# Performance work log

Measured on AMD Instinct MI355X. Metric: run time of the kernel, lower is better.

Reference implementation:

```python
import jax, jax.numpy as jnp
import numpy as np

HEADS = 7
DIM_HEAD = 64
SCALE = DIM_HEAD ** -0.5


def setup_inputs() -> dict:
    key = jax.random.key(0)
    ks = jax.random.split(key, 6)
    b, n, dim = 8, 1024, 448
    inner = HEADS * DIM_HEAD  # 448
    x = jax.random.normal(ks[0], (b, n, dim), dtype=jnp.float32)
    w_qv = jax.random.normal(ks[1], (dim, 2 * inner), dtype=jnp.float32) * 0.02
    ext_k = jax.random.normal(ks[2], (HEADS, n, DIM_HEAD), dtype=jnp.float32)
    ext_bias = jax.random.normal(ks[3], (HEADS, n, n), dtype=jnp.float32)
    w_out = jax.random.normal(ks[4], (inner, dim), dtype=jnp.float32) * 0.02
    b_out = jnp.zeros((dim,), dtype=jnp.float32)
    return {"x": x, "w_qv": w_qv, "ext_k": ext_k, "ext_bias": ext_bias,
            "w_out": w_out, "b_out": b_out}


def reference(x, w_qv, ext_k, ext_bias, w_out, b_out):
    b, n, dim = x.shape
    qv = x @ w_qv                                   # [b, n, 2*inner]
    q, v = jnp.split(qv, 2, axis=-1)
    # b n (h d) -> b h n d
    q = q.reshape(b, n, HEADS, DIM_HEAD).transpose(0, 2, 1, 3)
    v = v.reshape(b, n, HEADS, DIM_HEAD).transpose(0, 2, 1, 3)
    # scores vs external learned key, additive bias applied BEFORE scale
    dots = (jnp.einsum('bhnd,hmd->bhnm', q, ext_k) + ext_bias[None]) * SCALE
    attn = jax.nn.softmax(dots, axis=-1)
    out = jnp.einsum('bhnm,bhmd->bhnd', attn, v)
    out = out.transpose(0, 2, 1, 3).reshape(b, n, HEADS * DIM_HEAD)
    return out @ w_out + b_out  # dropout is identity in eval mode
```

## Files before the change

### kernel.cpp

```cpp
#include <hip/hip_runtime.h>
#include <hip/hip_bf16.h>
#include <hip/hip_fp16.h>

#define BATCH 8
#define NSEQ 1024
#define DIMM 448
#define NHEAD 7
#define HDIM 64
#define MROWS (BATCH*NSEQ)
#define KDIM 448
#define SCALE_F 0.125f

typedef short short8 __attribute__((ext_vector_type(8)));
typedef float floatx16 __attribute__((ext_vector_type(16)));

#define MFMA32(a,b,c) __builtin_amdgcn_mfma_f32_32x32x16_bf16(a,b,c,0,0,0)

__device__ __forceinline__ unsigned short f2bf(float f){
    __hip_bfloat16 h = __float2bfloat16(f);
    return *reinterpret_cast<unsigned short*>(&h);
}
__device__ __forceinline__ float bf2f(unsigned short u){
    __hip_bfloat16 h; *reinterpret_cast<unsigned short*>(&h) = u;
    return __bfloat162float(h);
}
__device__ __forceinline__ float h2f(unsigned short u){
    __half h; *reinterpret_cast<unsigned short*>(&h) = u;
    return __half2float(h);
}
__device__ __forceinline__ unsigned short f2h(float f){
    __half h = __float2half(f);
    return *reinterpret_cast<unsigned short*>(&h);
}

__global__ __launch_bounds__(256)
void prep_all(const float* __restrict__ x, const float* __restrict__ ek,
              const float* __restrict__ wqv, const float* __restrict__ wout,
              const float* __restrict__ eb,
              unsigned short* __restrict__ xh, unsigned short* __restrict__ ekh,
              unsigned short* __restrict__ wqvTh, unsigned short* __restrict__ woTh,
              unsigned short* __restrict__ woTl, unsigned short* __restrict__ bp)
{
    __shared__ float T[2][64][33];
    const int bx = blockIdx.x, tid = threadIdx.x;

    if (bx < 3584) {
        int i = bx*256 + tid;
        float4 v = ((const float4*)x)[i];
        ((ushort4*)xh)[i] = make_ushort4(f2bf(v.x), f2bf(v.y), f2bf(v.z), f2bf(v.w));
    } else if (bx < 4032) {
        int i = (bx-3584)*256 + tid;
        float4 v = ((const float4*)ek)[i];
        ((ushort4*)ekh)[i] = make_ushort4(f2bf(v.x), f2bf(v.y), f2bf(v.z), f2bf(v.w));
    } else if (bx < 4228) {
        int lid = (bx-4032)*4 + (tid>>6);
        int kc = lid % 56, ng = lid / 56;
        int n = ng*64 + (tid&63);
        unsigned short h[8];
#pragma unroll
        for (int j = 0; j < 8; ++j) h[j] = f2bf(wqv[(size_t)(kc*8+j)*896 + n]);
        size_t o = (size_t)n*KDIM + kc*8;
        *(ushort4*)(wqvTh + o)     = make_ushort4(h[0],h[1],h[2],h[3]);
        *(ushort4*)(wqvTh + o + 4) = make_ushort4(h[4],h[5],h[6],h[7]);
    } else if (bx < 4340) {
        int lid = (bx-4228)*4 + (tid>>6);
        int kc = lid % 56, ng = lid / 56;
        int n = ng*64 + (tid&63);
        ushort4 h0={0,0,0,0}, h1={0,0,0,0}, l0={0,0,0,0}, l1={0,0,0,0};
        if (n < DIMM) {
            unsigned short h[8], l[8];
#pragma unroll
            for (int j = 0; j < 8; ++j) {
                float f = wout[(size_t)(kc*8+j)*DIMM + n];
                h[j] = f2bf(f); l[j] = f2bf(f - bf2f(h[j]));
            }
            h0 = make_ushort4(h[0],h[1],h[2],h[3]); h1 = make_ushort4(h[4],h[5],h[6],h[7]);
            l0 = make_ushort4(l[0],l[1],l[2],l[3]); l1 = make_ushort4(l[4],l[5],l[6],l[7]);
        }
        size_t o = (size_t)n*KDIM + kc*8;
        *(ushort4*)(woTh + o) = h0; *(ushort4*)(woTh + o + 4) = h1;
        *(ushort4*)(woTl + o) = l0; *(ushort4*)(woTl + o + 4) = l1;
    } else {
        const int sub = tid >> 7, st = tid & 127;
        const int lid = (bx-4340)*2 + sub;
        const int mt = lid & 31, qt = (lid>>5) & 15, h = lid >> 9;
#pragma unroll
        for (int it = 0; it < 4; ++it) {
            int idx = it*128 + st;
            int row = idx >> 3, c4 = (idx & 7)*4;
            float4 v = *(const float4*)(eb + ((size_t)(h*NSEQ + qt*64 + row))*NSEQ + mt*32 + c4);
            T[sub][row][c4+0]=v.x; T[sub][row][c4+1]=v.y;
            T[sub][row][c4+2]=v.z; T[sub][row][c4+3]=v.w;
        }
        __syncthreads();
        const int g2 = st >> 6, lane = st & 63;
        const int lq = lane & 31, quad = lane >> 5;
        const int q = g2*32 + lq;
        unsigned short* dst = bp + ((((size_t)h*16 + qt)*32 + mt)*4 + g2*2)*512 + lane*8;
#pragma unroll
        for (int jj = 0; jj < 2; ++jj) {
            unsigned short o[8];
#pragma unroll
            for (int t = 0; t < 8; ++t) {
                int m = (t&3) + 8*(t>>2) + 16*jj + 4*quad;
                o[t] = f2h(T[sub][q][m] * SCALE_F);
            }
            *(ushort4*)(dst + jj*512)     = make_ushort4(o[0],o[1],o[2],o[3]);
            *(ushort4*)(dst + jj*512 + 4) = make_ushort4(o[4],o[5],o[6],o[7]);
        }
    }
}

__global__ __launch_bounds__(64, 2)
void gemm1_reg(const unsigned short* __restrict__ Ah, const unsigned short* __restrict__ Bh,
               unsigned short* __restrict__ qd, unsigned short* __restrict__ vTd)
{
    const int lane = threadIdx.x;
    const int lq = lane & 31, lh = lane >> 5;
    const int m0 = blockIdx.x * 64;
    const int y  = blockIdx.y;
    const int n0 = y * 64;
    const unsigned short* aB = Ah + (size_t)(m0 + lq)*KDIM + lh*8;
    const unsigned short* bB = Bh + (size_t)(n0 + lq)*KDIM + lh*8;

    floatx16 acc[2][2] = {};
    short8 aR[2][2][2], bR[2][2][2];
#define LD1(kt, par) {                                                        \
    _Pragma("unroll") for (int fm = 0; fm < 2; ++fm)                          \
    _Pragma("unroll") for (int c = 0; c < 2; ++c) {                           \
        aR[par][fm][c] = *(const short8*)(aB + (size_t)fm*32*KDIM + (kt)*32 + c*16); \
        bR[par][fm][c] = *(const short8*)(bB + (size_t)fm*32*KDIM + (kt)*32 + c*16); } }

    LD1(0, 0)
#pragma unroll
    for (int kt = 0; kt < 14; ++kt) {
        const int par = kt & 1;
        if (kt < 13) LD1(kt+1, par^1)
#pragma unroll
        for (int c = 0; c < 2; ++c)
#pragma unroll
            for (int fm = 0; fm < 2; ++fm)
#pragma unroll
                for (int fn = 0; fn < 2; ++fn)
                    acc[fm][fn] = MFMA32(aR[par][fm][c], bR[par][fn][c], acc[fm][fn]);
    }
#undef LD1

    if (y < NHEAD) {
#pragma unroll
        for (int fm = 0; fm < 2; ++fm)
#pragma unroll
            for (int fn = 0; fn < 2; ++fn) {
                const int d = fn*32 + lq;
#pragma unroll
                for (int r = 0; r < 16; ++r) {
                    const int gm = m0 + fm*32 + (r&3) + 8*(r>>2) + 4*lh;
                    const int b = gm >> 10, ns = gm & 1023;
                    qd[((size_t)((b*NHEAD + y)*NSEQ + ns))*HDIM + d] = f2bf(acc[fm][fn][r]);
                }
            }
    } else {
        const int head = y - NHEAD;
#pragma unroll
        for (int fm = 0; fm < 2; ++fm)
#pragma unroll
            for (int fn = 0; fn < 2; ++fn) {
                const int d = fn*32 + lq;
#pragma unroll
                for (int r = 0; r < 16; ++r) {
                    const int gm = m0 + fm*32 + (r&3) + 8*(r>>2) + 4*lh;
                    const int b = gm >> 10, ns = gm & 1023;
                    vTd[((size_t)((b*NHEAD + head)*HDIM + d))*NSEQ + ns] = f2bf(acc[fm][fn][r]);
                }
            }
    }
}

__global__ __launch_bounds__(64, 2)
void attn4(const unsigned short* __restrict__ qh_g, const unsigned short* __restrict__ vTh,
           const unsigned short* __restrict__ ekh, const unsigned short* __restrict__ bp,
           unsigned short* __restrict__ aoh, unsigned short* __restrict__ aol)
{
    __shared__ unsigned short pS[1024];
    __shared__ float linv[2][32];

    const int lane = threadIdx.x;
    const int lq = lane & 31, lh = lane >> 5;
    const int qt = blockIdx.x, head = blockIdx.y, b = blockIdx.z;
    const int bh = b*NHEAD + head;

    short8 qf[2][4];
#pragma unroll
    for (int g2 = 0; g2 < 2; ++g2)
#pragma unroll
        for (int c = 0; c < 4; ++c)
            qf[g2][c] = *(const short8*)(qh_g +
                ((size_t)(bh*NSEQ) + qt*64 + g2*32 + lq)*HDIM + c*16 + lh*8);

    const unsigned short* kB = ekh + ((size_t)head*NSEQ + lq)*HDIM + lh*8;
    const unsigned short* vB = vTh + ((size_t)(bh*HDIM) + lq)*NSEQ;
    const unsigned short* bB = bp + ((size_t)(head*16 + qt))*65536 + lane*8;

    short8 kR[2][4], vR[2][4], bR[2][4];
#define PREF(J, par) { const int mm = ((J) < 32) ? (J) : 0;                    \
    _Pragma("unroll") for (int c = 0; c < 4; ++c)                              \
        kR[par][c] = *(const short8*)(kB + (size_t)mm*2048 + c*16);            \
    _Pragma("unroll") for (int c2 = 0; c2 < 2; ++c2)                           \
    _Pragma("unroll") for (int h2 = 0; h2 < 2; ++h2)                           \
        vR[par][c2*2+h2] = *(const short8*)(vB + (size_t)(h2*32)*NSEQ + mm*32 + (c2*2+lh)*8); \
    _Pragma("unroll") for (int u = 0; u < 4; ++u)                              \
        bR[par][u] = *(const short8*)(bB + ((size_t)mm*4 + u)*512); }

    floatx16 O[2][2] = {};
    float ls[2] = {0.f, 0.f};

#define SEC(J, par, nxt) {                                                     \
    PREF((J)+1, nxt)                                                           \
    _Pragma("unroll") for (int g2 = 0; g2 < 2; ++g2) {                         \
        floatx16 S = {};                                                       \
        _Pragma("unroll") for (int c = 0; c < 4; ++c)                          \
            S = MFMA32(kR[par][c], qf[g2][c], S);                              \
        _Pragma("unroll") for (int g = 0; g < 4; ++g) {                        \
            unsigned short hb[4];                                              \
            _Pragma("unroll") for (int j2 = 0; j2 < 4; ++j2) {                 \
                const int i = g*4 + j2;                                        \
                float bs = h2f((unsigned short)bR[par][g2*2 + (i>>3)][i&7]);   \
                float pv = __expf(fmaf(S[i], SCALE_F, bs));                    \
                ls[g2] += pv;  hb[j2] = f2bf(pv);                              \
            }                                                                  \
            *(ushort4*)(pS + g*256 + lq*8 + lh*4) = make_ushort4(hb[0],hb[1],hb[2],hb[3]); \
        }                                                                      \
        _Pragma("unroll") for (int c2 = 0; c2 < 2; ++c2) {                     \
            short8 pf = *(const short8*)(pS + ((c2*2+lh)*32 + lq)*8);          \
            O[g2][0] = MFMA32(pf, vR[par][c2*2+0], O[g2][0]);                  \
            O[g2][1] = MFMA32(pf, vR[par][c2*2+1], O[g2][1]);                  \
        } } }

    PREF(0, 0)
    for (int jj = 0; jj < 16; ++jj) {
        SEC(2*jj,   0, 1)
        SEC(2*jj+1, 1, 0)
    }
#undef SEC
#undef PREF

    float lt0 = ls[0] + __shfl_xor(ls[0], 32);
    float lt1 = ls[1] + __shfl_xor(ls[1], 32);
    if (lh == 0) { linv[0][lq] = 1.f/lt0; linv[1][lq] = 1.f/lt1; }

#pragma unroll
    for (int g2 = 0; g2 < 2; ++g2)
#pragma unroll
        for (int r = 0; r < 16; ++r) {
            const int qr = (r&3) + 8*(r>>2) + 4*lh;
            const float inv = linv[g2][qr];
            const size_t o = ((size_t)(b*NSEQ) + qt*64 + g2*32 + qr)*DIMM + head*HDIM + lq;
            float v0 = O[g2][0][r]*inv, v1 = O[g2][1][r]*inv;
            unsigned short h0 = f2bf(v0), h1 = f2bf(v1);
            aoh[o]      = h0;  aol[o]      = f2bf(v0 - bf2f(h0));
            aoh[o + 32] = h1;  aol[o + 32] = f2bf(v1 - bf2f(h1));
        }
}

__global__ __launch_bounds__(64, 2)
void gemm2_reg(const unsigned short* __restrict__ Ah, const unsigned short* __restrict__ Al,
               const unsigned short* __restrict__ Bh, const unsigned short* __restrict__ Bl,
               const float* __restrict__ bias, float* __restrict__ out)
{
    const int lane = threadIdx.x;
    const int lq = lane & 31, lh = lane >> 5;
    const int m0 = blockIdx.x * 64;
    const int n0 = blockIdx.y * 64;
    const unsigned short* aBh = Ah + (size_t)(m0 + lq)*KDIM + lh*8;
    const unsigned short* aBl = Al + (size_t)(m0 + lq)*KDIM + lh*8;
    const unsigned short* bBh = Bh + (size_t)(n0 + lq)*KDIM + lh*8;
    const unsigned short* bBl = Bl + (size_t)(n0 + lq)*KDIM + lh*8;

    floatx16 acc[2][2] = {};
    short8 aH[2][2][2], aL[2][2][2], bH[2][2][2], bL[2][2][2];
#define LD2(kt, par) {                                                        \
    _Pragma("unroll") for (int fm = 0; fm < 2; ++fm)                          \
    _Pragma("unroll") for (int c = 0; c < 2; ++c) {                           \
        const size_t off = (size_t)fm*32*KDIM + (kt)*32 + c*16;               \
        aH[par][fm][c] = *(const short8*)(aBh + off);                         \
        aL[par][fm][c] = *(const short8*)(aBl + off);                         \
        bH[par][fm][c] = *(const short8*)(bBh + off);                         \
        bL[par][fm][c] = *(const short8*)(bBl + off); } }

    LD2(0, 0)
#pragma unroll
    for (int kt = 0; kt < 14; ++kt) {
        const int par = kt & 1;
        if (kt < 13) LD2(kt+1, par^1)
#pragma unroll
        for (int c = 0; c < 2; ++c)
#pragma unroll
            for (int fm = 0; fm < 2; ++fm)
#pragma unroll
                for (int fn = 0; fn < 2; ++fn) {
                    acc[fm][fn] = MFMA32(aH[par][fm][c], bH[par][fn][c], acc[fm][fn]);
                    acc[fm][fn] = MFMA32(aL[par][fm][c], bH[par][fn][c], acc[fm][fn]);
                    acc[fm][fn] = MFMA32(aH[par][fm][c], bL[par][fn][c], acc[fm][fn]);
                }
    }
#undef LD2

#pragma unroll
    for (int fm = 0; fm < 2; ++fm)
#pragma unroll
        for (int fn = 0; fn < 2; ++fn) {
            const int gn = n0 + fn*32 + lq;
            const float bv = bias[gn];
#pragma unroll
            for (int r = 0; r < 16; ++r) {
                const int gm = m0 + fm*32 + (r&3) + 8*(r>>2) + 4*lh;
                out[(size_t)gm*DIMM + gn] = acc[fm][fn][r] + bv;
            }
        }
}

extern "C" void kernel_launch(void* const* d_in, const int* in_sizes, int n_in,
                              void* d_out, int out_size, void* d_ws, size_t ws_size,
                              hipStream_t stream)
{
    const float* x    = (const float*)d_in[0];
    const float* wqv  = (const float*)d_in[1];
    const float* ek   = (const float*)d_in[2];
    const float* eb   = (const float*)d_in[3];
    const float* wout = (const float*)d_in[4];
    const float* bout = (const float*)d_in[5];
    float* out = (float*)d_out;

    const size_t MK = (size_t)MROWS*KDIM;
    const size_t EK = (size_t)NHEAD*NSEQ*HDIM;
    unsigned short* p = (unsigned short*)d_ws;
    unsigned short* xh    = p;  p += MK;
    unsigned short* wqvTh = p;  p += (size_t)896*KDIM;
    unsigned short* woTh  = p;  p += (size_t)512*KDIM;
    unsigned short* woTl  = p;  p += (size_t)512*KDIM;
    unsigned short* ekh   = p;  p += EK;
    unsigned short* qh    = p;  p += MK;
    unsigned short* vTh   = p;  p += MK;
    unsigned short* bp    = p;  p += (size_t)NHEAD*NSEQ*NSEQ;
    unsigned short* aoh   = p;  p += MK;
    unsigned short* aol   = p;  p += MK;

    prep_all<<<6132, 256, 0, stream>>>(x, ek, wqv, wout, eb,
                                       xh, ekh, wqvTh, woTh, woTl, bp);
    gemm1_reg<<<dim3(128, 14), 64, 0, stream>>>(xh, wqvTh, qh, vTh);
    attn4<<<dim3(16, NHEAD, BATCH), 64, 0, stream>>>(qh, vTh, ekh, bp, aoh, aol);
    gemm2_reg<<<dim3(128, 7), 64, 0, stream>>>(aoh, aol, woTh, woTl, bout, out);
}
```

Baseline: 200.6 us.

## Rewrite pipeline: fuse bias prepack and x conversion, batch-share bias in attention

Drops the separate fp16 repacking pass over the large bias tensor and the x-to-bf16 conversion. gemm1 now converts fp32 x on the fly and prescales q by scale*log2e. The attention kernel puts all 8 batches of one head in a single 512-thread block so each bias row is read once from fp32 memory and shared across batches. It also uses exp2 and moves P between lane halves with cross-lane shuffles instead of shared memory. Both GEMMs move to 4-wave 128x128 tiles, which trades occupancy and adds padding waste in gemm2 (448 columns do not fill 4x128).

```diff
diff --git a/kernel.cpp b/kernel.cpp
--- a/kernel.cpp
+++ b/kernel.cpp
@@ -1,6 +1,5 @@
 #include <hip/hip_runtime.h>
 #include <hip/hip_bf16.h>
-#include <hip/hip_fp16.h>
 
 #define BATCH 8
 #define NSEQ 1024
@@ -9,10 +8,12 @@
 #define HDIM 64
 #define MROWS (BATCH*NSEQ)
 #define KDIM 448
-#define SCALE_F 0.125f
+#define CB 0.18033688f
 
 typedef short short8 __attribute__((ext_vector_type(8)));
+typedef int   int4v  __attribute__((ext_vector_type(4)));
 typedef float floatx16 __attribute__((ext_vector_type(16)));
+typedef unsigned int u32;
 
 #define MFMA32(a,b,c) __builtin_amdgcn_mfma_f32_32x32x16_bf16(a,b,c,0,0,0)
 
@@ -24,36 +25,23 @@
     __hip_bfloat16 h; *reinterpret_cast<unsigned short*>(&h) = u;
     return __bfloat162float(h);
 }
-__device__ __forceinline__ float h2f(unsigned short u){
-    __half h; *reinterpret_cast<unsigned short*>(&h) = u;
-    return __half2float(h);
-}
-__device__ __forceinline__ unsigned short f2h(float f){
-    __half h = __float2half(f);
-    return *reinterpret_cast<unsigned short*>(&h);
+__device__ __forceinline__ short8 i4_to_s8(int4v v){
+    union { int4v i; short8 s; } u; u.i = v; return u.s;
 }
 
 __global__ __launch_bounds__(256)
-void prep_all(const float* __restrict__ x, const float* __restrict__ ek,
-              const float* __restrict__ wqv, const float* __restrict__ wout,
-              const float* __restrict__ eb,
-              unsigned short* __restrict__ xh, unsigned short* __restrict__ ekh,
-              unsigned short* __restrict__ wqvTh, unsigned short* __restrict__ woTh,
-              unsigned short* __restrict__ woTl, unsigned short* __restrict__ bp)
-{
-    __shared__ float T[2][64][33];
+void prep_r8(const float* __restrict__ ek, const float* __restrict__ wqv,
+             const float* __restrict__ wout,
+             unsigned short* __restrict__ ekh, unsigned short* __restrict__ wqvTh,
+             unsigned short* __restrict__ woTh, unsigned short* __restrict__ woTl)
+{
     const int bx = blockIdx.x, tid = threadIdx.x;
-
-    if (bx < 3584) {
+    if (bx < 448) {
         int i = bx*256 + tid;
-        float4 v = ((const float4*)x)[i];
-        ((ushort4*)xh)[i] = make_ushort4(f2bf(v.x), f2bf(v.y), f2bf(v.z), f2bf(v.w));
-    } else if (bx < 4032) {
-        int i = (bx-3584)*256 + tid;
         float4 v = ((const float4*)ek)[i];
         ((ushort4*)ekh)[i] = make_ushort4(f2bf(v.x), f2bf(v.y), f2bf(v.z), f2bf(v.w));
-    } else if (bx < 4228) {
-        int lid = (bx-4032)*4 + (tid>>6);
+    } else if (bx < 644) {
+        int lid = (bx-448)*4 + (tid>>6);
         int kc = lid % 56, ng = lid / 56;
         int n = ng*64 + (tid&63);
         unsigned short h[8];
@@ -62,8 +50,8 @@
         size_t o = (size_t)n*KDIM + kc*8;
         *(ushort4*)(wqvTh + o)     = make_ushort4(h[0],h[1],h[2],h[3]);
         *(ushort4*)(wqvTh + o + 4) = make_ushort4(h[4],h[5],h[6],h[7]);
-    } else if (bx < 4340) {
-        int lid = (bx-4228)*4 + (tid>>6);
+    } else {
+        int lid = (bx-644)*4 + (tid>>6);
         int kc = lid % 56, ng = lid / 56;
         int n = ng*64 + (tid&63);
         ushort4 h0={0,0,0,0}, h1={0,0,0,0}, l0={0,0,0,0}, l1={0,0,0,0};
@@ -80,163 +68,140 @@
         size_t o = (size_t)n*KDIM + kc*8;
         *(ushort4*)(woTh + o) = h0; *(ushort4*)(woTh + o + 4) = h1;
         *(ushort4*)(woTl + o) = l0; *(ushort4*)(woTl + o + 4) = l1;
-    } else {
-        const int sub = tid >> 7, st = tid & 127;
-        const int lid = (bx-4340)*2 + sub;
-        const int mt = lid & 31, qt = (lid>>5) & 15, h = lid >> 9;
-#pragma unroll
-        for (int it = 0; it < 4; ++it) {
-            int idx = it*128 + st;
-            int row = idx >> 3, c4 = (idx & 7)*4;
-            float4 v = *(const float4*)(eb + ((size_t)(h*NSEQ + qt*64 + row))*NSEQ + mt*32 + c4);
-            T[sub][row][c4+0]=v.x; T[sub][row][c4+1]=v.y;
-            T[sub][row][c4+2]=v.z; T[sub][row][c4+3]=v.w;
+    }
+}
+
+__global__ __launch_bounds__(256, 2)
+void gemm1_r8(const float* __restrict__ x, const unsigned short* __restrict__ Bh,
+              unsigned short* __restrict__ qd, unsigned short* __restrict__ vTd)
+{
+    const int tid = threadIdx.x, w = tid >> 6, lane = tid & 63;
+    const int lq = lane & 31, lh = lane >> 5;
+    const int m0 = blockIdx.x*128 + w*32, n0 = blockIdx.y*128;
+    const float* aB = x + (size_t)(m0 + lq)*KDIM + lh*8;
+    const unsigned short* bB = Bh + (size_t)(n0 + lq)*KDIM + lh*8;
+
+    floatx16 acc[4] = {};
+    float4 aF[2][2][2];
+    short8 bR[2][8];
+#define LD1(kt, sl) {                                                          \
+    _Pragma("unroll") for (int c = 0; c < 2; ++c) {                            \
+        aF[sl][c][0] = *(const float4*)(aB + (kt)*32 + c*16);                  \
+        aF[sl][c][1] = *(const float4*)(aB + (kt)*32 + c*16 + 4);              \
+        _Pragma("unroll") for (int fn = 0; fn < 4; ++fn)                       \
+            bR[sl][fn*2+c] = *(const short8*)(bB + (size_t)(fn*32)*KDIM + (kt)*32 + c*16); } }
+
+    LD1(0, 0)
+#pragma unroll
+    for (int kt = 0; kt < 14; ++kt) {
+        if (kt < 13) LD1(kt+1, (kt+1)&1)
+        const int sl = kt & 1;
+#pragma unroll
+        for (int c = 0; c < 2; ++c) {
+            float4 f0 = aF[sl][c][0], f1 = aF[sl][c][1];
+            short8 a;
+            a[0]=(short)f2bf(f0.x); a[1]=(short)f2bf(f0.y);
+            a[2]=(short)f2bf(f0.z); a[3]=(short)f2bf(f0.w);
+            a[4]=(short)f2bf(f1.x); a[5]=(short)f2bf(f1.y);
+            a[6]=(short)f2bf(f1.z); a[7]=(short)f2bf(f1.w);
+#pragma unroll
+            for (int fn = 0; fn < 4; ++fn)
+                acc[fn] = MFMA32(a, bR[sl][fn*2+c], acc[fn]);
         }
-        __syncthreads();
-        const int g2 = st >> 6, lane = st & 63;
-        const int lq = lane & 31, quad = lane >> 5;
-        const int q = g2*32 + lq;
-        unsigned short* dst = bp + ((((size_t)h*16 + qt)*32 + mt)*4 + g2*2)*512 + lane*8;
-#pragma unroll
-        for (int jj = 0; jj < 2; ++jj) {
-            unsigned short o[8];
-#pragma unroll
-            for (int t = 0; t < 8; ++t) {
-                int m = (t&3) + 8*(t>>2) + 16*jj + 4*quad;
-                o[t] = f2h(T[sub][q][m] * SCALE_F);
-            }
-            *(ushort4*)(dst + jj*512)     = make_ushort4(o[0],o[1],o[2],o[3]);
-            *(ushort4*)(dst + jj*512 + 4) = make_ushort4(o[4],o[5],o[6],o[7]);
+    }
+#undef LD1
+
+#pragma unroll
+    for (int fn = 0; fn < 4; ++fn) {
+        const int gn = n0 + fn*32 + lq;
+        const int hcol = gn >> 6, d = gn & 63;
+#pragma unroll
+        for (int r = 0; r < 16; ++r) {
+            const int gm = m0 + (r&3) + 8*(r>>2) + 4*lh;
+            const int b = gm >> 10, ns = gm & 1023;
+            if (hcol < NHEAD)
+                qd[((size_t)((b*NHEAD + hcol)*NSEQ + ns))*HDIM + d] = f2bf(acc[fn][r]*CB);
+            else
+                vTd[((size_t)((b*NHEAD + hcol - NHEAD)*HDIM + d))*NSEQ + ns] = f2bf(acc[fn][r]);
         }
     }
 }
 
-__global__ __launch_bounds__(64, 2)
-void gemm1_reg(const unsigned short* __restrict__ Ah, const unsigned short* __restrict__ Bh,
-               unsigned short* __restrict__ qd, unsigned short* __restrict__ vTd)
-{
-    const int lane = threadIdx.x;
+__global__ __launch_bounds__(512, 2)
+void attn6(const unsigned short* __restrict__ qh_g, const unsigned short* __restrict__ vTh,
+           const unsigned short* __restrict__ ekh, const float* __restrict__ eb,
+           unsigned short* __restrict__ aoh, unsigned short* __restrict__ aol)
+{
+    __shared__ float linv[8][32];
+
+    const int tid = threadIdx.x;
+    const int w = tid >> 6;
+    const int lane = tid & 63;
     const int lq = lane & 31, lh = lane >> 5;
-    const int m0 = blockIdx.x * 64;
-    const int y  = blockIdx.y;
-    const int n0 = y * 64;
-    const unsigned short* aB = Ah + (size_t)(m0 + lq)*KDIM + lh*8;
-    const unsigned short* bB = Bh + (size_t)(n0 + lq)*KDIM + lh*8;
-
-    floatx16 acc[2][2] = {};
-    short8 aR[2][2][2], bR[2][2][2];
-#define LD1(kt, par) {                                                        \
-    _Pragma("unroll") for (int fm = 0; fm < 2; ++fm)                          \
-    _Pragma("unroll") for (int c = 0; c < 2; ++c) {                           \
-        aR[par][fm][c] = *(const short8*)(aB + (size_t)fm*32*KDIM + (kt)*32 + c*16); \
-        bR[par][fm][c] = *(const short8*)(bB + (size_t)fm*32*KDIM + (kt)*32 + c*16); } }
-
-    LD1(0, 0)
-#pragma unroll
-    for (int kt = 0; kt < 14; ++kt) {
-        const int par = kt & 1;
-        if (kt < 13) LD1(kt+1, par^1)
-#pragma unroll
-        for (int c = 0; c < 2; ++c)
-#pragma unroll
-            for (int fm = 0; fm < 2; ++fm)
-#pragma unroll
-                for (int fn = 0; fn < 2; ++fn)
-                    acc[fm][fn] = MFMA32(aR[par][fm][c], bR[par][fn][c], acc[fm][fn]);
-    }
-#undef LD1
-
-    if (y < NHEAD) {
-#pragma unroll
-        for (int fm = 0; fm < 2; ++fm)
-#pragma unroll
-            for (int fn = 0; fn < 2; ++fn) {
-                const int d = fn*32 + lq;
-#pragma unroll
-                for (int r = 0; r < 16; ++r) {
-                    const int gm = m0 + fm*32 + (r&3) + 8*(r>>2) + 4*lh;
-                    const int b = gm >> 10, ns = gm & 1023;
-                    qd[((size_t)((b*NHEAD + y)*NSEQ + ns))*HDIM + d] = f2bf(acc[fm][fn][r]);
-                }
-            }
-    } else {
-        const int head = y - NHEAD;
-#pragma unroll
-        for (int fm = 0; fm < 2; ++fm)
-#pragma unroll
-            for (int fn = 0; fn < 2; ++fn) {
-                const int d = fn*32 + lq;
-#pragma unroll
-                for (int r = 0; r < 16; ++r) {
-                    const int gm = m0 + fm*32 + (r&3) + 8*(r>>2) + 4*lh;
-                    const int b = gm >> 10, ns = gm & 1023;
-                    vTd[((size_t)((b*NHEAD + head)*HDIM + d))*NSEQ + ns] = f2bf(acc[fm][fn][r]);
-                }
-            }
-    }
-}
-
-__global__ __launch_bounds__(64, 2)
-void attn4(const unsigned short* __restrict__ qh_g, const unsigned short* __restrict__ vTh,
-           const unsigned short* __restrict__ ekh, const unsigned short* __restrict__ bp,
-           unsigned short* __restrict__ aoh, unsigned short* __restrict__ aol)
-{
-    __shared__ unsigned short pS[1024];
-    __shared__ float linv[2][32];
-
-    const int lane = threadIdx.x;
-    const int lq = lane & 31, lh = lane >> 5;
-    const int qt = blockIdx.x, head = blockIdx.y, b = blockIdx.z;
-    const int bh = b*NHEAD + head;
-
-    short8 qf[2][4];
-#pragma unroll
-    for (int g2 = 0; g2 < 2; ++g2)
-#pragma unroll
-        for (int c = 0; c < 4; ++c)
-            qf[g2][c] = *(const short8*)(qh_g +
-                ((size_t)(bh*NSEQ) + qt*64 + g2*32 + lq)*HDIM + c*16 + lh*8);
-
-    const unsigned short* kB = ekh + ((size_t)head*NSEQ + lq)*HDIM + lh*8;
+    const int qt = blockIdx.x, h = blockIdx.y;
+    const int bh = w*NHEAD + h;
+
+    short8 qf[4];
+#pragma unroll
+    for (int c = 0; c < 4; ++c)
+        qf[c] = *(const short8*)(qh_g +
+            ((size_t)(bh*NSEQ) + qt*32 + lq)*HDIM + c*16 + lh*8);
+
+    const unsigned short* kB = ekh + ((size_t)h*NSEQ + lq)*HDIM + lh*8;
     const unsigned short* vB = vTh + ((size_t)(bh*HDIM) + lq)*NSEQ;
-    const unsigned short* bB = bp + ((size_t)(head*16 + qt))*65536 + lane*8;
-
-    short8 kR[2][4], vR[2][4], bR[2][4];
-#define PREF(J, par) { const int mm = ((J) < 32) ? (J) : 0;                    \
+    const float* bB = eb + ((size_t)(h*NSEQ) + qt*32 + lq)*NSEQ;
+
+    short8 kR[2][4], vR[2][4];
+    float4 bR[2][4];
+#define PREF(MM, SL) {                                                         \
     _Pragma("unroll") for (int c = 0; c < 4; ++c)                              \
-        kR[par][c] = *(const short8*)(kB + (size_t)mm*2048 + c*16);            \
+        kR[SL][c] = *(const short8*)(kB + (size_t)(MM)*2048 + c*16);           \
+    _Pragma("unroll") for (int fn = 0; fn < 2; ++fn)                           \
     _Pragma("unroll") for (int c2 = 0; c2 < 2; ++c2)                           \
-    _Pragma("unroll") for (int h2 = 0; h2 < 2; ++h2)                           \
-        vR[par][c2*2+h2] = *(const short8*)(vB + (size_t)(h2*32)*NSEQ + mm*32 + (c2*2+lh)*8); \
-    _Pragma("unroll") for (int u = 0; u < 4; ++u)                              \
-        bR[par][u] = *(const short8*)(bB + ((size_t)mm*4 + u)*512); }
-
-    floatx16 O[2][2] = {};
-    float ls[2] = {0.f, 0.f};
-
-#define SEC(J, par, nxt) {                                                     \
-    PREF((J)+1, nxt)                                                           \
-    _Pragma("unroll") for (int g2 = 0; g2 < 2; ++g2) {                         \
-        floatx16 S = {};                                                       \
-        _Pragma("unroll") for (int c = 0; c < 4; ++c)                          \
-            S = MFMA32(kR[par][c], qf[g2][c], S);                              \
-        _Pragma("unroll") for (int g = 0; g < 4; ++g) {                        \
-            unsigned short hb[4];                                              \
-            _Pragma("unroll") for (int j2 = 0; j2 < 4; ++j2) {                 \
-                const int i = g*4 + j2;                                        \
-                float bs = h2f((unsigned short)bR[par][g2*2 + (i>>3)][i&7]);   \
-                float pv = __expf(fmaf(S[i], SCALE_F, bs));                    \
-                ls[g2] += pv;  hb[j2] = f2bf(pv);                              \
-            }                                                                  \
-            *(ushort4*)(pS + g*256 + lq*8 + lh*4) = make_ushort4(hb[0],hb[1],hb[2],hb[3]); \
+        vR[SL][fn*2+c2] = __builtin_nontemporal_load(                          \
+            (const short8*)(vB + (size_t)(fn*32)*NSEQ + (MM)*32 + c2*16 + lh*8)); \
+    _Pragma("unroll") for (int g = 0; g < 4; ++g)                              \
+        bR[SL][g] = *(const float4*)(bB + (size_t)(MM)*32 + g*8 + lh*4); }
+
+    floatx16 O[2] = {};
+    float ls = 0.f;
+
+#define SEC(J, PAR, NXT) {                                                     \
+    { const int mm_ = ((J)+1 < 32) ? (J)+1 : 0; PREF(mm_, NXT) }               \
+    floatx16 S = {};                                                           \
+    S = MFMA32(kR[PAR][0], qf[0], S);                                          \
+    S = MFMA32(kR[PAR][1], qf[1], S);                                          \
+    S = MFMA32(kR[PAR][2], qf[2], S);                                          \
+    S = MFMA32(kR[PAR][3], qf[3], S);                                          \
+    u32 Pq[4][2];                                                              \
+    _Pragma("unroll") for (int g = 0; g < 4; ++g) {                            \
+        float bvv[4] = {bR[PAR][g].x, bR[PAR][g].y, bR[PAR][g].z, bR[PAR][g].w}; \
+        unsigned short hb[4];                                                  \
+        _Pragma("unroll") for (int j = 0; j < 4; ++j) {                        \
+            float pv = __builtin_amdgcn_exp2f(fmaf(bvv[j], CB, S[g*4+j]));     \
+            ls += pv;  hb[j] = f2bf(pv);                                       \
         }                                                                      \
-        _Pragma("unroll") for (int c2 = 0; c2 < 2; ++c2) {                     \
-            short8 pf = *(const short8*)(pS + ((c2*2+lh)*32 + lq)*8);          \
-            O[g2][0] = MFMA32(pf, vR[par][c2*2+0], O[g2][0]);                  \
-            O[g2][1] = MFMA32(pf, vR[par][c2*2+1], O[g2][1]);                  \
-        } } }
+        Pq[g][0] = (u32)hb[0] | ((u32)hb[1] << 16);                            \
+        Pq[g][1] = (u32)hb[2] | ((u32)hb[3] << 16);                            \
+    }                                                                          \
+    u32 pp[4][2];                                                              \
+    _Pragma("unroll") for (int g = 0; g < 4; ++g) {                            \
+        pp[g][0] = (u32)__shfl_xor((int)Pq[g][0], 32);                         \
+        pp[g][1] = (u32)__shfl_xor((int)Pq[g][1], 32);                         \
+    }                                                                          \
+    _Pragma("unroll") for (int c2 = 0; c2 < 2; ++c2) {                         \
+        int4v iv;                                                              \
+        iv.x = lh ? (int)pp[2*c2+1][0] : (int)Pq[2*c2][0];                     \
+        iv.y = lh ? (int)pp[2*c2+1][1] : (int)Pq[2*c2][1];                     \
+        iv.z = lh ? (int)Pq[2*c2+1][0] : (int)pp[2*c2][0];                     \
+        iv.w = lh ? (int)Pq[2*c2+1][1] : (int)pp[2*c2][1];                     \
+        short8 af = i4_to_s8(iv);                                              \
+        O[0] = MFMA32(af, vR[PAR][0*2+c2], O[0]);                              \
+        O[1] = MFMA32(af, vR[PAR][1*2+c2], O[1]);                              \
+    } }
 
     PREF(0, 0)
+#pragma unroll
     for (int jj = 0; jj < 16; ++jj) {
         SEC(2*jj,   0, 1)
         SEC(2*jj+1, 1, 0)
@@ -244,79 +209,73 @@
 #undef SEC
 #undef PREF
 
-    float lt0 = ls[0] + __shfl_xor(ls[0], 32);
-    float lt1 = ls[1] + __shfl_xor(ls[1], 32);
-    if (lh == 0) { linv[0][lq] = 1.f/lt0; linv[1][lq] = 1.f/lt1; }
-
-#pragma unroll
-    for (int g2 = 0; g2 < 2; ++g2)
-#pragma unroll
-        for (int r = 0; r < 16; ++r) {
-            const int qr = (r&3) + 8*(r>>2) + 4*lh;
-            const float inv = linv[g2][qr];
-            const size_t o = ((size_t)(b*NSEQ) + qt*64 + g2*32 + qr)*DIMM + head*HDIM + lq;
-            float v0 = O[g2][0][r]*inv, v1 = O[g2][1][r]*inv;
-            unsigned short h0 = f2bf(v0), h1 = f2bf(v1);
-            aoh[o]      = h0;  aol[o]      = f2bf(v0 - bf2f(h0));
-            aoh[o + 32] = h1;  aol[o + 32] = f2bf(v1 - bf2f(h1));
-        }
-}
-
-__global__ __launch_bounds__(64, 2)
-void gemm2_reg(const unsigned short* __restrict__ Ah, const unsigned short* __restrict__ Al,
-               const unsigned short* __restrict__ Bh, const unsigned short* __restrict__ Bl,
-               const float* __restrict__ bias, float* __restrict__ out)
-{
-    const int lane = threadIdx.x;
+    float lt = ls + __shfl_xor(ls, 32);
+    if (lh == 0) linv[w][lq] = 1.0f / lt;
+
+    const size_t obase = ((size_t)(w*NSEQ) + qt*32)*DIMM + h*HDIM;
+#pragma unroll
+    for (int r = 0; r < 16; ++r) {
+        const int qr = (r&3) + 8*(r>>2) + 4*lh;
+        const float inv = linv[w][qr];
+        float v0 = O[0][r]*inv, v1 = O[1][r]*inv;
+        unsigned short h0 = f2bf(v0), h1 = f2bf(v1);
+        size_t o = obase + (size_t)qr*DIMM + lq;
+        aoh[o]      = h0;  aol[o]      = f2bf(v0 - bf2f(h0));
+        aoh[o + 32] = h1;  aol[o + 32] = f2bf(v1 - bf2f(h1));
+    }
+}
+
+__global__ __launch_bounds__(256, 1)
+void gemm2_r8(const unsigned short* __restrict__ Ah, const unsigned short* __restrict__ Al,
+              const unsigned short* __restrict__ Bh, const unsigned short* __restrict__ Bl,
+              const float* __restrict__ bias, float* __restrict__ out)
+{
+    const int tid = threadIdx.x, w = tid >> 6, lane = tid & 63;
     const int lq = lane & 31, lh = lane >> 5;
-    const int m0 = blockIdx.x * 64;
-    const int n0 = blockIdx.y * 64;
-    const unsigned short* aBh = Ah + (size_t)(m0 + lq)*KDIM + lh*8;
-    const unsigned short* aBl = Al + (size_t)(m0 + lq)*KDIM + lh*8;
-    const unsigned short* bBh = Bh + (size_t)(n0 + lq)*KDIM + lh*8;
-    const unsigned short* bBl = Bl + (size_t)(n0 + lq)*KDIM + lh*8;
-
-    floatx16 acc[2][2] = {};
-    short8 aH[2][2][2], aL[2][2][2], bH[2][2][2], bL[2][2][2];
-#define LD2(kt, par) {                                                        \
-    _Pragma("unroll") for (int fm = 0; fm < 2; ++fm)                          \
-    _Pragma("unroll") for (int c = 0; c < 2; ++c) {                           \
-        const size_t off = (size_t)fm*32*KDIM + (kt)*32 + c*16;               \
-        aH[par][fm][c] = *(const short8*)(aBh + off);                         \
-        aL[par][fm][c] = *(const short8*)(aBl + off);                         \
-        bH[par][fm][c] = *(const short8*)(bBh + off);                         \
-        bL[par][fm][c] = *(const short8*)(bBl + off); } }
+    const int m0 = blockIdx.x*128 + w*32, n0 = blockIdx.y*128;
+    const unsigned short* aHB = Ah + (size_t)(m0 + lq)*KDIM + lh*8;
+    const unsigned short* aLB = Al + (size_t)(m0 + lq)*KDIM + lh*8;
+    const unsigned short* bHB = Bh + (size_t)(n0 + lq)*KDIM + lh*8;
+    const unsigned short* bLB = Bl + (size_t)(n0 + lq)*KDIM + lh*8;
+
+    floatx16 acc[4] = {};
+    short8 aH[2][2], aL[2][2], bH[2][8], bL[2][8];
+#define LD2(kt, sl) {                                                          \
+    _Pragma("unroll") for (int c = 0; c < 2; ++c) {                            \
+        aH[sl][c] = *(const short8*)(aHB + (kt)*32 + c*16);                    \
+        aL[sl][c] = *(const short8*)(aLB + (kt)*32 + c*16);                    \
+        _Pragma("unroll") for (int fn = 0; fn < 4; ++fn) {                     \
+            bH[sl][fn*2+c] = *(const short8*)(bHB + (size_t)(fn*32)*KDIM + (kt)*32 + c*16); \
+            bL[sl][fn*2+c] = *(const short8*)(bLB + (size_t)(fn*32)*KDIM + (kt)*32 + c*16); } } }
 
     LD2(0, 0)
 #pragma unroll
     for (int kt = 0; kt < 14; ++kt) {
-        const int par = kt & 1;
-        if (kt < 13) LD2(kt+1, par^1)
+        if (kt < 13) LD2(kt+1, (kt+1)&1)
+        const int sl = kt & 1;
 #pragma unroll
         for (int c = 0; c < 2; ++c)
 #pragma unroll
-            for (int fm = 0; fm < 2; ++fm)
-#pragma unroll
-                for (int fn = 0; fn < 2; ++fn) {
-                    acc[fm][fn] = MFMA32(aH[par][fm][c], bH[par][fn][c], acc[fm][fn]);
-                    acc[fm][fn] = MFMA32(aL[par][fm][c], bH[par][fn][c], acc[fm][fn]);
-                    acc[fm][fn] = MFMA32(aH[par][fm][c], bL[par][fn][c], acc[fm][fn]);
-                }
+            for (int fn = 0; fn < 4; ++fn) {
+                acc[fn] = MFMA32(aH[sl][c], bH[sl][fn*2+c], acc[fn]);
+                acc[fn] = MFMA32(aL[sl][c], bH[sl][fn*2+c], acc[fn]);
+                acc[fn] = MFMA32(aH[sl][c], bL[sl][fn*2+c], acc[fn]);
+            }
     }
 #undef LD2
 
 #pragma unroll
-    for (int fm = 0; fm < 2; ++fm)
-#pragma unroll
-        for (int fn = 0; fn < 2; ++fn) {
-            const int gn = n0 + fn*32 + lq;
+    for (int fn = 0; fn < 4; ++fn) {
+        const int gn = n0 + fn*32 + lq;
+        if (gn < DIMM) {
             const float bv = bias[gn];
 #pragma unroll
             for (int r = 0; r < 16; ++r) {
-                const int gm = m0 + fm*32 + (r&3) + 8*(r>>2) + 4*lh;
-                out[(size_t)gm*DIMM + gn] = acc[fm][fn][r] + bv;
+                const int gm = m0 + (r&3) + 8*(r>>2) + 4*lh;
+                out[(size_t)gm*DIMM + gn] = acc[fn][r] + bv;
             }
         }
+    }
 }
 
 extern "C" void kernel_launch(void* const* d_in, const int* in_sizes, int n_in,
@@ -334,20 +293,17 @@
     const size_t MK = (size_t)MROWS*KDIM;
     const size_t EK = (size_t)NHEAD*NSEQ*HDIM;
     unsigned short* p = (unsigned short*)d_ws;
-    unsigned short* xh    = p;  p += MK;
+    unsigned short* ekh   = p;  p += EK;
     unsigned short* wqvTh = p;  p += (size_t)896*KDIM;
     unsigned short* woTh  = p;  p += (size_t)512*KDIM;
     unsigned short* woTl  = p;  p += (size_t)512*KDIM;
-    unsigned short* ekh   = p;  p += EK;
     unsigned short* qh    = p;  p += MK;
     unsigned short* vTh   = p;  p += MK;
-    unsigned short* bp    = p;  p += (size_t)NHEAD*NSEQ*NSEQ;
     unsigned short* aoh   = p;  p += MK;
     unsigned short* aol   = p;  p += MK;
 
-    prep_all<<<6132, 256, 0, stream>>>(x, ek, wqv, wout, eb,
-                                       xh, ekh, wqvTh, woTh, woTl, bp);
-    gemm1_reg<<<dim3(128, 14), 64, 0, stream>>>(xh, wqvTh, qh, vTh);
-    attn4<<<dim3(16, NHEAD, BATCH), 64, 0, stream>>>(qh, vTh, ekh, bp, aoh, aol);
-    gemm2_reg<<<dim3(128, 7), 64, 0, stream>>>(aoh, aol, woTh, woTl, bout, out);
-}
+    prep_r8<<<756, 256, 0, stream>>>(ek, wqv, wout, ekh, wqvTh, woTh, woTl);
+    gemm1_r8<<<dim3(64, 7), 256, 0, stream>>>(x, wqvTh, qh, vTh);
+    attn6<<<dim3(32, NHEAD), 512, 0, stream>>>(qh, vTh, ekh, eb, aoh, aol);
+    gemm2_r8<<<dim3(64, 4), 256, 0, stream>>>(aoh, aol, woTh, woTl, bout, out);
+}
```

Result: slower. 291.3 us (+45.2%).
